# Kernel optimization log

Measured on AMD Instinct MI355X. Metric: run time of the kernel, lower is better.

Reference implementation:

```python
import jax, jax.numpy as jnp
import numpy as np

CIN, COUT, R, N, B = 4, 4, 4, 4096, 32

def setup_inputs() -> dict:
    key = jax.random.key(0)
    k1, k2, k3 = jax.random.split(key, 3)
    x = jax.random.normal(k1, (CIN, B, N), dtype=jnp.float32)
    # torch.nn.init.normal(std=0.01)
    G = 0.01 * jax.random.normal(k2, (CIN, COUT, R, N), dtype=jnp.float32)
    H = 0.01 * jax.random.normal(k3, (CIN, COUT, R, N), dtype=jnp.float32)
    return {"x": x, "G": G, "H": H}

def reference(x, G, H):
    """LDR layer, displacement='toep_corner' (cycle=True).

    For each channel pair (i,j):
        M_ij = sum_s C_1(G[i,j,s]) @ C_{-1}(H[i,j,s])^T
    where C_f(v) is the f-circulant matrix with first column v
    (= Krylov matrix of the f-unit-circulant shift Z_f with vector v).
    out[j] = sum_i M_ij @ x[i]^T  (batched over batch dim).

    Identities used (F = DFT):
      C_1(u) y      = ifft(fft(u) * fft(y))
      C_1(u)^T y    = fft(fft(u) * ifft(y))
      C_f(v)        = D^{-1} C_1(D v) D,  D = diag(zeta^k), zeta = f^{1/n}
      => C_{-1}(h)^T y = D * fft(fft(D*h) * ifft(conj(D)*y)), D_k = exp(i*pi*k/n)
    All channel pairs and ranks are batched in a single FFT call (no Python
    loops over channels, unlike the original double loop).
    """
    cin, b, n = x.shape
    k = jnp.arange(n)
    D = jnp.exp(1j * jnp.pi * k / n).astype(jnp.complex64)   # zeta^k for f=-1
    Dinv = jnp.conj(D)

    # --- step 1: t[i,j,s,b,:] = C_{-1}(H[i,j,s])^T x[i,b,:]  -> (cin,cout,r,b,n)
    Hf = jnp.fft.fft(D * H.astype(jnp.complex64), axis=-1)           # (cin,cout,r,n)
    Xf = jnp.fft.ifft(Dinv * x.astype(jnp.complex64), axis=-1)       # (cin,b,n)
    t = D * jnp.fft.fft(Hf[:, :, :, None, :] * Xf[:, None, None, :, :], axis=-1)

    # --- step 2: out[j,b,:] = Re ifft( sum_{i,s} fft(G[i,j,s]) * fft(t[i,j,s,b]) )
    Gf = jnp.fft.fft(G, axis=-1).astype(jnp.complex64)               # (cin,cout,r,n)
    Tf = jnp.fft.fft(t, axis=-1)                                     # (cin,cout,r,b,n)
    Yf = jnp.einsum('ijsn,ijsbn->jbn', Gf, Tf)                       # (cout,b,n)
    return jnp.real(jnp.fft.ifft(Yf, axis=-1)).astype(x.dtype)
```

## Files before the change

kernel.cpp:

```cpp
#include <hip/hip_runtime.h>
#include <hip/hip_fp16.h>
#include <math.h>


#define NFFT  4096
#define NT    256
#define CIN   4
#define COUT  4
#define RANK  4
#define BATCH 32
#define PI_F  3.14159265358979323846f

constexpr float CP16[16] = {
    1.0000000000000000f,  0.9807852804032304f,  0.9238795325112867f,  0.8314696123025452f,
    0.7071067811865476f,  0.5555702330196022f,  0.3826834323650898f,  0.1950903220161282f,
    0.0000000000000000f, -0.1950903220161282f, -0.3826834323650898f, -0.5555702330196022f,
   -0.7071067811865476f, -0.8314696123025452f, -0.9238795325112867f, -0.9807852804032304f };
constexpr float SP16[16] = {
    0.0000000000000000f,  0.1950903220161282f,  0.3826834323650898f,  0.5555702330196022f,
    0.7071067811865476f,  0.8314696123025452f,  0.9238795325112867f,  0.9807852804032304f,
    1.0000000000000000f,  0.9807852804032304f,  0.9238795325112867f,  0.8314696123025452f,
    0.7071067811865476f,  0.5555702330196022f,  0.3826834323650898f,  0.1950903220161282f };

__device__ __forceinline__ float2 cmul(float2 a, float2 b) {
    return make_float2(a.x*b.x - a.y*b.y, a.x*b.y + a.y*b.x);
}
__device__ __forceinline__ float2 cadd(float2 a, float2 b){ return make_float2(a.x+b.x, a.y+b.y); }
__device__ __forceinline__ float2 csub(float2 a, float2 b){ return make_float2(a.x-b.x, a.y-b.y); }

__device__ __forceinline__ int SW(int e){ return e ^ ((e >> 4) & 15); }

template<int SIGN>
__device__ __forceinline__ void dft16(float2 v[16]) {
    const float sgn = (float)SIGN;
    const float C8 = 0.923879532511287f, S8 = 0.382683432365090f, H2 = 0.707106781186548f;
    const float2 w1 = make_float2( C8,  sgn*S8);
    const float2 w2 = make_float2( H2,  sgn*H2);
    const float2 w3 = make_float2( S8,  sgn*C8);
    const float2 w4 = make_float2(0.f,  sgn);
    const float2 w6 = make_float2(-H2,  sgn*H2);
    const float2 w9 = make_float2(-C8, -sgn*S8);
    float2 t[16];
    #pragma unroll
    for (int p = 0; p < 4; ++p) {
        float2 a0 = v[p], a1 = v[p+4], a2 = v[p+8], a3 = v[p+12];
        float2 b0 = cadd(a0,a2), b1 = csub(a0,a2), b2 = cadd(a1,a3), b3 = csub(a1,a3);
        float2 ib3 = make_float2(-sgn*b3.y, sgn*b3.x);
        float2 X0 = cadd(b0,b2), X2c = csub(b0,b2);
        float2 X1 = cadd(b1,ib3), X3 = csub(b1,ib3);
        if (p == 1) { X1 = cmul(X1,w1); X2c = cmul(X2c,w2); X3 = cmul(X3,w3); }
        else if (p == 2) { X1 = cmul(X1,w2); X2c = cmul(X2c,w4); X3 = cmul(X3,w6); }
        else if (p == 3) { X1 = cmul(X1,w3); X2c = cmul(X2c,w6); X3 = cmul(X3,w9); }
        t[4*p+0]=X0; t[4*p+1]=X1; t[4*p+2]=X2c; t[4*p+3]=X3;
    }
    #pragma unroll
    for (int q = 0; q < 4; ++q) {
        float2 a0 = t[q], a1 = t[q+4], a2 = t[q+8], a3 = t[q+12];
        float2 b0 = cadd(a0,a2), b1 = csub(a0,a2), b2 = cadd(a1,a3), b3 = csub(a1,a3);
        float2 ib3 = make_float2(-sgn*b3.y, sgn*b3.x);
        v[q+0]  = cadd(b0,b2);
        v[q+8]  = csub(b0,b2);
        v[q+4]  = cadd(b1,ib3);
        v[q+12] = csub(b1,ib3);
    }
}

__device__ __forceinline__ void twiddle16(float2 v[16], float ang) {
    float sn, cs; __sincosf(ang, &sn, &cs);
    float2 w  = make_float2(cs, sn);
    float2 w2 = cmul(w, w);
    float2 to = w;
    float2 te = w2;
    v[1] = cmul(v[1], to);
    v[2] = cmul(v[2], te);
    #pragma unroll
    for (int k = 3; k < 16; k += 2) {
        to = cmul(to, w2); v[k] = cmul(v[k], to);
        if (k + 1 < 16) { te = cmul(te, w2); v[k+1] = cmul(v[k+1], te); }
    }
}

template<int SIGN>
__device__ void fft4096_r16(float2 v[16], float2* lds, int tid) {
    dft16<SIGN>(v);
    twiddle16(v, (float)SIGN * 2.0f * PI_F * (float)tid / 4096.0f);
    #pragma unroll
    for (int k = 0; k < 16; ++k) lds[SW(16*tid + k)] = v[k];
    __syncthreads();
    #pragma unroll
    for (int r = 0; r < 16; ++r) v[r] = lds[SW(tid + 256*r)];
    dft16<SIGN>(v);
    twiddle16(v, (float)SIGN * 2.0f * PI_F * (float)(tid >> 4) / 256.0f);
    __syncthreads();
    {
        const int q = tid & 15, p = tid >> 4;
        #pragma unroll
        for (int k = 0; k < 16; ++k) lds[SW(q + 256*p + 16*k)] = v[k];
    }
    __syncthreads();
    #pragma unroll
    for (int r = 0; r < 16; ++r) v[r] = lds[SW(tid + 256*r)];
    dft16<SIGN>(v);
    __syncthreads();
}

__global__ __launch_bounds__(NT, 2) void ldr_pre_k(
    const float* __restrict__ x, const float* __restrict__ G, const float* __restrict__ H,
    float2* __restrict__ Hc, float2* __restrict__ Gf, float2* __restrict__ Xf)
{
    __shared__ float2 lds[NFFT];
    const int tid = threadIdx.x;
    const int bid = blockIdx.x;
    float2 v[16];
    if (bid < 32) {
        const float* h0 = H + (size_t)(2*bid)     * NFFT;
        const float* h1 = H + (size_t)(2*bid + 1) * NFFT;
        float sn, cs; __sincosf(PI_F * (float)tid / (float)NFFT, &sn, &cs);
        const float2 dt = make_float2(cs, sn);
        #pragma unroll
        for (int k = 0; k < 16; ++k) {
            const int e = tid + 256*k;
            const float2 d = cmul(dt, make_float2(CP16[k], SP16[k]));
            v[k] = cmul(d, make_float2(h0[e], h1[e]));
        }
        fft4096_r16<-1>(v, lds, tid);
        float2* o = Hc + (size_t)bid * NFFT;
        #pragma unroll
        for (int k = 0; k < 16; ++k) o[tid + 256*k] = v[k];
    } else if (bid < 96) {
        const int row = bid - 32;
        const float* g = G + (size_t)row * NFFT;
        #pragma unroll
        for (int k = 0; k < 16; ++k) v[k] = make_float2(g[tid + 256*k], 0.0f);
        fft4096_r16<-1>(v, lds, tid);
        float2* o = Gf + (size_t)row * NFFT;
        #pragma unroll
        for (int k = 0; k < 16; ++k) o[tid + 256*k] = v[k];
    } else {
        const int row = bid - 96;
        const float* xp = x + (size_t)row * NFFT;
        float sn, cs; __sincosf(PI_F * (float)tid / (float)NFFT, &sn, &cs);
        const float2 dt = make_float2(cs, -sn);
        #pragma unroll
        for (int k = 0; k < 16; ++k) {
            const int e = tid + 256*k;
            const float2 d = cmul(dt, make_float2(CP16[k], -SP16[k]));
            float xv = xp[e];
            v[k] = make_float2(d.x*xv, d.y*xv);
        }
        fft4096_r16<1>(v, lds, tid);
        const float invn = 1.0f / (float)NFFT;
        float2* o = Xf + (size_t)row * NFFT;
        #pragma unroll
        for (int k = 0; k < 16; ++k) o[tid + 256*k] = make_float2(v[k].x*invn, v[k].y*invn);
    }
}

__global__ __launch_bounds__(NT, 3) void ldr_mid_k(
    const float2* __restrict__ Hc, const float2* __restrict__ Xf,
    const float2* __restrict__ Gf, __half2* __restrict__ Ph)
{
    __shared__ float2 lds[NFFT];
    const int tid = threadIdx.x;
    const int bid = blockIdx.x;
    const int b   = bid & (BATCH - 1);
    const int ip  = bid >> 5;
    const int pr  = ip & 1;
    const int ij  = ip >> 1;
    const int i   = ij >> 2;
    const int j   = ij & 3;
    const int r0  = ij*RANK + 2*pr;
    const float2* xrow = Xf + (size_t)(i*BATCH + b) * NFFT;
    const float2* hc = Hc + (size_t)ip * NFFT;
    const float2* g0 = Gf + (size_t)r0 * NFFT;
    const float2* g1 = g0 + NFFT;

    float2 v[16];
    #pragma unroll
    for (int k = 0; k < 16; ++k) {
        const int e = tid + 256*k;
        v[k] = cmul(hc[e], xrow[e]);
    }
    fft4096_r16<-1>(v, lds, tid);
    {
        float sn, cs; __sincosf(PI_F * (float)tid / (float)NFFT, &sn, &cs);
        const float2 dt = make_float2(cs, sn);
        #pragma unroll
        for (int k = 0; k < 16; ++k) {
            const float2 d = cmul(dt, make_float2(CP16[k], SP16[k]));
            v[k] = cmul(v[k], d);
        }
    }
    fft4096_r16<-1>(v, lds, tid);

    #pragma unroll
    for (int k = 8; k < 16; ++k) lds[SW(tid + 256*k)] = v[k];
    __syncthreads();

    const int u = i*2 + pr;
    __half2* prow = Ph + (size_t)((u*COUT + j)*BATCH + b) * (NFFT/2);
    #pragma unroll
    for (int k = 0; k < 8; ++k) {
        const int e = tid + 256*k;
        const float2 Zk = v[k];
        float2 Zm;
        if (e == 0) Zm = Zk;
        else        Zm = lds[SW(4096 - e)];
        const float2 V1 = make_float2(0.5f*(Zk.x + Zm.x), 0.5f*(Zk.y - Zm.y));
        const float2 V2 = make_float2(0.5f*(Zk.y + Zm.y), 0.5f*(Zm.x - Zk.x));
        float2 Y = cadd(cmul(g0[e], V1), cmul(g1[e], V2));
        if (k == 0 && tid == 0) {
            const float2 Zn = v[8];
            const float Ynyq = g0[2048].x * Zn.x + g1[2048].x * Zn.y;
            Y = make_float2(Y.x, Ynyq);
        }
        prow[e] = __floats2half2_rn(Y.x, Y.y);
    }
}

__global__ __launch_bounds__(NT, 2) void ldr_fin_k(
    const __half2* __restrict__ Ph, float* __restrict__ out)
{
    __shared__ float2 lds[NFFT];
    __shared__ float2 sh[NFFT/2];
    const int tid = threadIdx.x;
    const int bid = blockIdx.x;
    const int b = bid & (BATCH - 1);
    const int j = bid >> 5;

    float2 a[8];
    #pragma unroll
    for (int k = 0; k < 8; ++k) a[k] = make_float2(0.f, 0.f);
    #pragma unroll
    for (int u = 0; u < 8; ++u) {
        const int4* row4 = (const int4*)(Ph + (size_t)((u*COUT + j)*BATCH + b) * (NFFT/2));
        #pragma unroll
        for (int c = 0; c < 2; ++c) {
            const int4 w = row4[tid + 256*c];
            const int ww[4] = { w.x, w.y, w.z, w.w };
            #pragma unroll
            for (int r = 0; r < 4; ++r) {
                __half2 h = *(const __half2*)&ww[r];
                float2 f = __half22float2(h);
                a[c*4+r] = cadd(a[c*4+r], f);
            }
        }
    }
    float4* sh4 = (float4*)sh;
    #pragma unroll
    for (int c = 0; c < 2; ++c) {
        sh4[2*(tid + 256*c) + 0] = make_float4(a[c*4+0].x, a[c*4+0].y, a[c*4+1].x, a[c*4+1].y);
        sh4[2*(tid + 256*c) + 1] = make_float4(a[c*4+2].x, a[c*4+2].y, a[c*4+3].x, a[c*4+3].y);
    }
    __syncthreads();

    const float dc  = sh[0].x;
    const float nyq = sh[0].y;
    float2 v[16];
    #pragma unroll
    for (int k = 0; k < 8; ++k) v[k] = sh[tid + 256*k];
    if (tid == 0) v[0] = make_float2(dc, 0.0f);
    #pragma unroll
    for (int k = 8; k < 16; ++k) {
        const int m = 4096 - (tid + 256*k);
        if (m == 2048) {
            v[k] = make_float2(nyq, 0.0f);
        } else {
            float2 c = sh[m];
            v[k] = make_float2(c.x, -c.y);
        }
    }
    fft4096_r16<1>(v, lds, tid);
    const float invn = 1.0f / (float)NFFT;
    float* orow = out + (size_t)bid * NFFT;
    #pragma unroll
    for (int k = 0; k < 16; ++k) orow[tid + 256*k] = v[k].x * invn;
}

extern "C" void kernel_launch(void* const* d_in, const int* in_sizes, int n_in,
                              void* d_out, int out_size, void* d_ws, size_t ws_size,
                              hipStream_t stream) {
    const float* x = (const float*)d_in[0];
    const float* G = (const float*)d_in[1];
    const float* H = (const float*)d_in[2];
    float* out = (float*)d_out;

    float2*  Hc = (float2*)d_ws;
    float2*  Gf = Hc + (size_t)32 * NFFT;
    float2*  Xf = Gf + (size_t)64 * NFFT;
    __half2* Ph = (__half2*)(Xf + (size_t)128 * NFFT);

    ldr_pre_k<<<224, NT, 0, stream>>>(x, G, H, Hc, Gf, Xf);
    ldr_mid_k<<<CIN * COUT * RANK * BATCH / 2, NT, 0, stream>>>(Hc, Xf, Gf, Ph);
    ldr_fin_k<<<COUT * BATCH, NT, 0, stream>>>(Ph, out);
}
```

Before: 108.2 us.

## Use 512-thread radix-8 FFT in mid kernel to cut register pressure

The middle kernel now uses a four-pass radix-8 4096-point FFT with 512 threads per block instead of a three-pass radix-16 FFT with 256 threads. Each thread holds 8 complex values instead of 16, which lowers register use and should raise wave occupancy and latency hiding. In exchange there is an extra LDS round trip and barrier per FFT and more twiddle computations.

```diff
diff --git a/kernel.cpp b/kernel.cpp
--- a/kernel.cpp
+++ b/kernel.cpp
@@ -5,6 +5,7 @@
 
 #define NFFT  4096
 #define NT    256
+#define NTM   512
 #define CIN   4
 #define COUT  4
 #define RANK  4
@@ -21,6 +22,12 @@
     0.7071067811865476f,  0.8314696123025452f,  0.9238795325112867f,  0.9807852804032304f,
     1.0000000000000000f,  0.9807852804032304f,  0.9238795325112867f,  0.8314696123025452f,
     0.7071067811865476f,  0.5555702330196022f,  0.3826834323650898f,  0.1950903220161282f };
+constexpr float CP8[8] = {
+    1.0000000000000000f,  0.9238795325112867f,  0.7071067811865476f,  0.3826834323650898f,
+    0.0000000000000000f, -0.3826834323650898f, -0.7071067811865476f, -0.9238795325112867f };
+constexpr float SP8[8] = {
+    0.0000000000000000f,  0.3826834323650898f,  0.7071067811865476f,  0.9238795325112867f,
+    1.0000000000000000f,  0.9238795325112867f,  0.7071067811865476f,  0.3826834323650898f };
 
 __device__ __forceinline__ float2 cmul(float2 a, float2 b) {
     return make_float2(a.x*b.x - a.y*b.y, a.x*b.y + a.y*b.x);
@@ -101,6 +108,79 @@
     #pragma unroll
     for (int r = 0; r < 16; ++r) v[r] = lds[SW(tid + 256*r)];
     dft16<SIGN>(v);
+    __syncthreads();
+}
+
+template<int SIGN>
+__device__ __forceinline__ void dft8(float2 v[8]) {
+    const float sgn = (float)SIGN;
+    const float H2 = 0.707106781186548f;
+    float2 a0 = v[0], a1 = v[2], a2 = v[4], a3 = v[6];
+    float2 b0 = cadd(a0,a2), b1 = csub(a0,a2), b2 = cadd(a1,a3), b3 = csub(a1,a3);
+    float2 ib3 = make_float2(-sgn*b3.y, sgn*b3.x);
+    float2 E0 = cadd(b0,b2), E2 = csub(b0,b2), E1 = cadd(b1,ib3), E3 = csub(b1,ib3);
+    a0 = v[1]; a1 = v[3]; a2 = v[5]; a3 = v[7];
+    b0 = cadd(a0,a2); b1 = csub(a0,a2); b2 = cadd(a1,a3); b3 = csub(a1,a3);
+    ib3 = make_float2(-sgn*b3.y, sgn*b3.x);
+    float2 O0 = cadd(b0,b2), O2 = csub(b0,b2), O1 = cadd(b1,ib3), O3 = csub(b1,ib3);
+    const float2 w1 = make_float2( H2,  sgn*H2);
+    const float2 w3 = make_float2(-H2,  sgn*H2);
+    O1 = cmul(O1, w1);
+    O2 = make_float2(-sgn*O2.y, sgn*O2.x);
+    O3 = cmul(O3, w3);
+    v[0] = cadd(E0,O0); v[4] = csub(E0,O0);
+    v[1] = cadd(E1,O1); v[5] = csub(E1,O1);
+    v[2] = cadd(E2,O2); v[6] = csub(E2,O2);
+    v[3] = cadd(E3,O3); v[7] = csub(E3,O3);
+}
+
+__device__ __forceinline__ void twiddle8(float2 v[8], float ang) {
+    float sn, cs; __sincosf(ang, &sn, &cs);
+    float2 w  = make_float2(cs, sn);
+    float2 w2 = cmul(w, w);
+    float2 to = w;
+    float2 te = w2;
+    v[1] = cmul(v[1], to);
+    v[2] = cmul(v[2], te);
+    to = cmul(to, w2); v[3] = cmul(v[3], to);
+    te = cmul(te, w2); v[4] = cmul(v[4], te);
+    to = cmul(to, w2); v[5] = cmul(v[5], to);
+    te = cmul(te, w2); v[6] = cmul(v[6], te);
+    to = cmul(to, w2); v[7] = cmul(v[7], to);
+}
+
+template<int SIGN>
+__device__ void fft4096_r8(float2 v[8], float2* lds, int tid) {
+    dft8<SIGN>(v);
+    twiddle8(v, (float)SIGN * 2.0f * PI_F * (float)tid / 4096.0f);
+    #pragma unroll
+    for (int k = 0; k < 8; ++k) lds[SW(8*tid + k)] = v[k];
+    __syncthreads();
+    #pragma unroll
+    for (int r = 0; r < 8; ++r) v[r] = lds[SW(tid + 512*r)];
+    dft8<SIGN>(v);
+    twiddle8(v, (float)SIGN * 2.0f * PI_F * (float)(tid >> 3) / 512.0f);
+    __syncthreads();
+    {
+        const int base = (tid & 7) + 64*(tid >> 3);
+        #pragma unroll
+        for (int k = 0; k < 8; ++k) lds[SW(base + 8*k)] = v[k];
+    }
+    __syncthreads();
+    #pragma unroll
+    for (int r = 0; r < 8; ++r) v[r] = lds[SW(tid + 512*r)];
+    dft8<SIGN>(v);
+    twiddle8(v, (float)SIGN * 2.0f * PI_F * (float)(tid >> 6) / 64.0f);
+    __syncthreads();
+    {
+        const int base = (tid & 63) + 512*(tid >> 6);
+        #pragma unroll
+        for (int k = 0; k < 8; ++k) lds[SW(base + 64*k)] = v[k];
+    }
+    __syncthreads();
+    #pragma unroll
+    for (int r = 0; r < 8; ++r) v[r] = lds[SW(tid + 512*r)];
+    dft8<SIGN>(v);
     __syncthreads();
 }
 
@@ -156,7 +236,7 @@
     }
 }
 
-__global__ __launch_bounds__(NT, 3) void ldr_mid_k(
+__global__ __launch_bounds__(NTM, 2) void ldr_mid_k(
     const float2* __restrict__ Hc, const float2* __restrict__ Xf,
     const float2* __restrict__ Gf, __half2* __restrict__ Ph)
 {
@@ -170,38 +250,38 @@
     const int i   = ij >> 2;
     const int j   = ij & 3;
     const int r0  = ij*RANK + 2*pr;
+    const float2* hc   = Hc + (size_t)ip * NFFT;
     const float2* xrow = Xf + (size_t)(i*BATCH + b) * NFFT;
-    const float2* hc = Hc + (size_t)ip * NFFT;
-    const float2* g0 = Gf + (size_t)r0 * NFFT;
-    const float2* g1 = g0 + NFFT;
-
-    float2 v[16];
-    #pragma unroll
-    for (int k = 0; k < 16; ++k) {
-        const int e = tid + 256*k;
+    const float2* g0   = Gf + (size_t)r0 * NFFT;
+    const float2* g1   = g0 + NFFT;
+    const int u = i*2 + pr;
+
+    float2 v[8];
+    #pragma unroll
+    for (int k = 0; k < 8; ++k) {
+        const int e = tid + NTM*k;
         v[k] = cmul(hc[e], xrow[e]);
     }
-    fft4096_r16<-1>(v, lds, tid);
+    fft4096_r8<-1>(v, lds, tid);
     {
         float sn, cs; __sincosf(PI_F * (float)tid / (float)NFFT, &sn, &cs);
         const float2 dt = make_float2(cs, sn);
         #pragma unroll
-        for (int k = 0; k < 16; ++k) {
-            const float2 d = cmul(dt, make_float2(CP16[k], SP16[k]));
+        for (int k = 0; k < 8; ++k) {
+            const float2 d = cmul(dt, make_float2(CP8[k], SP8[k]));
             v[k] = cmul(v[k], d);
         }
     }
-    fft4096_r16<-1>(v, lds, tid);
-
-    #pragma unroll
-    for (int k = 8; k < 16; ++k) lds[SW(tid + 256*k)] = v[k];
-    __syncthreads();
-
-    const int u = i*2 + pr;
+    fft4096_r8<-1>(v, lds, tid);
+
+    #pragma unroll
+    for (int k = 4; k < 8; ++k) lds[SW(tid + NTM*k)] = v[k];
+    __syncthreads();
+
     __half2* prow = Ph + (size_t)((u*COUT + j)*BATCH + b) * (NFFT/2);
     #pragma unroll
-    for (int k = 0; k < 8; ++k) {
-        const int e = tid + 256*k;
+    for (int k = 0; k < 4; ++k) {
+        const int e = tid + NTM*k;
         const float2 Zk = v[k];
         float2 Zm;
         if (e == 0) Zm = Zk;
@@ -210,7 +290,7 @@
         const float2 V2 = make_float2(0.5f*(Zk.y + Zm.y), 0.5f*(Zm.x - Zk.x));
         float2 Y = cadd(cmul(g0[e], V1), cmul(g1[e], V2));
         if (k == 0 && tid == 0) {
-            const float2 Zn = v[8];
+            const float2 Zn = v[4];
             const float Ynyq = g0[2048].x * Zn.x + g1[2048].x * Zn.y;
             Y = make_float2(Y.x, Ynyq);
         }
@@ -291,6 +371,6 @@
     __half2* Ph = (__half2*)(Xf + (size_t)128 * NFFT);
 
     ldr_pre_k<<<224, NT, 0, stream>>>(x, G, H, Hc, Gf, Xf);
-    ldr_mid_k<<<CIN * COUT * RANK * BATCH / 2, NT, 0, stream>>>(Hc, Xf, Gf, Ph);
+    ldr_mid_k<<<CIN * COUT * RANK * BATCH / 2, NTM, 0, stream>>>(Hc, Xf, Gf, Ph);
     ldr_fin_k<<<COUT * BATCH, NT, 0, stream>>>(Ph, out);
 }
```

New measurement: 98.34 us. 1.1x faster.
